# Optimization experiments

Measured on AMD Instinct MI355X. Metric: run time of the kernel, lower is better.

Reference implementation:

```python
import jax, jax.numpy as jnp
import numpy as np

B, NK, NQ = 16, 1024, 1024
D_IN, D_V, D_H = 3, 8, 128
NUGGET = 1e-3   # diagonal regularizer for the kriging covariance solve
EPS = 1e-12     # keeps sqrt differentiable at zero distance


def _mlp(x, w1, b1, w2, b2, w3, b3):
    # Linear -> ReLU -> Linear -> ReLU -> Linear (torch Linear: y = x @ W.T + b)
    h = jax.nn.relu(x @ w1.T + b1)
    h = jax.nn.relu(h @ w2.T + b2)
    return h @ w3.T + b3


def _cdist(a, b):
    # a: [B,N,D], b: [B,M,D] -> [B,N,M] Euclidean distances
    d2 = (jnp.sum(a * a, -1)[:, :, None]
          + jnp.sum(b * b, -1)[:, None, :]
          - 2.0 * jnp.einsum('bnd,bmd->bnm', a, b))
    return jnp.sqrt(jnp.maximum(d2, 0.0) + EPS)


def _linear_init(key, out_f, in_f):
    k1, k2 = jax.random.split(key)
    lim = 1.0 / np.sqrt(in_f)
    w = jax.random.uniform(k1, (out_f, in_f), jnp.float32, -lim, lim)
    b = jax.random.uniform(k2, (out_f,), jnp.float32, -lim, lim)
    return w, b


def setup_inputs() -> dict:
    key = jax.random.key(0)
    ks = jax.random.split(key, 10)
    KEY = jax.random.normal(ks[0], (B, NK, D_IN), jnp.float32)
    VALUE = jax.random.normal(ks[1], (B, NK, D_V), jnp.float32)
    QUERY = jax.random.normal(ks[2], (B, NQ, D_IN), jnp.float32)
    W1_w, W1_b = _linear_init(ks[3], D_H, D_IN)
    W2_w, W2_b = _linear_init(ks[4], D_H, D_H)
    W3_w, W3_b = _linear_init(ks[5], D_IN, D_H)
    Wv1_w, Wv1_b = _linear_init(ks[6], D_H, D_V)
    Wv2_w, Wv2_b = _linear_init(ks[7], D_H, D_H)
    Wv3_w, Wv3_b = _linear_init(ks[8], D_V, D_H)
    return dict(KEY=KEY, VALUE=VALUE, QUERY=QUERY,
                W1_w=W1_w, W1_b=W1_b, W2_w=W2_w, W2_b=W2_b, W3_w=W3_w, W3_b=W3_b,
                Wv1_w=Wv1_w, Wv1_b=Wv1_b, Wv2_w=Wv2_w, Wv2_b=Wv2_b, Wv3_w=Wv3_w, Wv3_b=Wv3_b)


def reference(KEY, VALUE, QUERY,
              W1_w, W1_b, W2_w, W2_b, W3_w, W3_b,
              Wv1_w, Wv1_b, Wv2_w, Wv2_b, Wv3_w, Wv3_b):
    # shared MLP on KEY and QUERY, separate MLP on VALUE
    Wk = _mlp(KEY, W1_w, W1_b, W2_w, W2_b, W3_w, W3_b)
    Wq = _mlp(QUERY, W1_w, W1_b, W2_w, W2_b, W3_w, W3_b)
    Wv = _mlp(VALUE, Wv1_w, Wv1_b, Wv2_w, Wv2_b, Wv3_w, Wv3_b)
    VALUE_scale = VALUE * Wv                  # einsum('bij,bij->bij')
    # kriging prediction with learned elementwise coordinate scalings
    Ks = KEY * Wk                             # [B,NK,D_IN]
    Qs = QUERY * Wq                           # [B,NQ,D_IN]
    C_kk = jnp.exp(-_cdist(Ks, Ks)) + NUGGET * jnp.eye(NK, dtype=KEY.dtype)  # [B,NK,NK]
    C_qk = jnp.exp(-_cdist(Qs, Ks))                                          # [B,NQ,NK]
    # kriging weights: solve C_kk @ lam = C_qk^T  -> lam [B,NK,NQ]
    lam = jnp.linalg.solve(C_kk, jnp.swapaxes(C_qk, 1, 2))
    # prediction: weighted sum of scaled values -> [B,NQ,D_V]
    return jnp.einsum('bkq,bkv->bqv', lam, VALUE_scale)
```

## Files before the change

### kernel.cpp

```cpp
#include <hip/hip_runtime.h>
#include <hip/hip_bf16.h>


__device__ __forceinline__ int row_of(int e) {
    int i = (int)((sqrtf(8.0f * (float)e + 1.0f) - 1.0f) * 0.5f);
    while ((i + 1) * (i + 2) / 2 <= e) i++;
    while (i * (i + 1) / 2 > e) i--;
    return i;
}

__global__ void k_transpose(const float* __restrict__ W2, const float* __restrict__ Wv2,
                            float* __restrict__ W2T, float* __restrict__ Wv2T) {
    int tid = blockIdx.x * 256 + threadIdx.x;
    int e = tid & 16383;
    int r = e >> 7, c = e & 127;
    if (tid < 16384) W2T[c * 128 + r] = W2[e];
    else             Wv2T[c * 128 + r] = Wv2[e];
}

template<int DI, int P>
__device__ __forceinline__ void mlp_body(const float* __restrict__ in,
                                         float* __restrict__ out, int base,
                                         const float* __restrict__ W1,
                                         const float* __restrict__ b1,
                                         const float* __restrict__ W2T,
                                         const float* __restrict__ b2,
                                         const float* __restrict__ W3,
                                         const float* __restrict__ b3) {
    __shared__ float xs[P][DI];
    __shared__ float h1[P][128];
    __shared__ float h2[P][129];
    int t = threadIdx.x;
    for (int i = t; i < P * DI; i += 128) xs[i / DI][i % DI] = in[base * DI + i];
    __syncthreads();
    float w1r[DI];
#pragma unroll
    for (int d = 0; d < DI; d++) w1r[d] = W1[t * DI + d];
    float b1t = b1[t], b2t = b2[t];
#pragma unroll
    for (int p = 0; p < P; p++) {
        float s = b1t;
#pragma unroll
        for (int d = 0; d < DI; d++) s += w1r[d] * xs[p][d];
        h1[p][t] = fmaxf(s, 0.0f);
    }
    __syncthreads();
    float acc[P];
#pragma unroll
    for (int p = 0; p < P; p++) acc[p] = b2t;
    for (int k = 0; k < 128; k++) {
        float w = W2T[k * 128 + t];
#pragma unroll
        for (int p = 0; p < P; p++) acc[p] += w * h1[p][k];
    }
#pragma unroll
    for (int p = 0; p < P; p++) h2[p][t] = fmaxf(acc[p], 0.0f);
    __syncthreads();
    if (t < P * DI) {
        int p = t / DI, d = t % DI;
        float s = b3[d];
        for (int k = 0; k < 128; k++) s += W3[d * 128 + k] * h2[p][k];
        int gi = base * DI + t;
        out[gi] = in[gi] * s;
    }
}

__global__ void k_mlp_kq(const float* __restrict__ KEY, float* __restrict__ Ks,
                         const float* __restrict__ QUERY, float* __restrict__ Qs,
                         const float* __restrict__ W1, const float* __restrict__ b1,
                         const float* __restrict__ W2T, const float* __restrict__ b2,
                         const float* __restrict__ W3, const float* __restrict__ b3) {
    if (blockIdx.x < 512)
        mlp_body<3, 32>(KEY, Ks, blockIdx.x * 32, W1, b1, W2T, b2, W3, b3);
    else
        mlp_body<3, 32>(QUERY, Qs, (blockIdx.x - 512) * 32, W1, b1, W2T, b2, W3, b3);
}

__global__ void k_mlp_v(const float* __restrict__ VALUE, float* __restrict__ Vs,
                        const float* __restrict__ W1, const float* __restrict__ b1,
                        const float* __restrict__ W2T, const float* __restrict__ b2,
                        const float* __restrict__ W3, const float* __restrict__ b3) {
    mlp_body<8, 16>(VALUE, Vs, blockIdx.x * 16, W1, b1, W2T, b2, W3, b3);
}

__global__ void k_buildC(const float* __restrict__ Ks, float* __restrict__ C) {
    long idx = (long)blockIdx.x * 256 + threadIdx.x;
    int b = (int)(idx >> 20);
    int rem = (int)(idx & 1048575);
    int i = rem >> 10, j = rem & 1023;
    const float* a = Ks + ((long)b * 1024 + i) * 3;
    const float* bb = Ks + ((long)b * 1024 + j) * 3;
    float d0 = a[0] - bb[0], d1 = a[1] - bb[1], d2 = a[2] - bb[2];
    float dist = sqrtf(d0 * d0 + d1 * d1 + d2 * d2 + 1e-12f);
    float v = __expf(-dist);
    if (i == j) v += 1e-3f;
    C[idx] = v;
}

__device__ void potf_body(float* __restrict__ C, float* __restrict__ V,
                          float* smem, int o, int last, int b) {
    int tid = threadIdx.x;
    float* A = C + (long)b * 1048576;
    float* Vp = V + (long)b * 8192;
    float (*T)[132]      = (float(*)[132])smem;
    float (*cv)[8]       = (float(*)[8])(smem + 16896);
    float (*cw)[8]       = (float(*)[8])(smem + 17920);
    float (*Pn)[8]       = (float(*)[8])(smem + 18944);
    float (*St)[32][132] = (float(*)[32][132])(smem + 19968);
    float (*Lc)[32][33]  = (float(*)[32][33])(smem + 19968);
    float* rsd           = smem + 28416;
    float (*Wb)[32][36]  = (float(*)[32][36])(smem + 28544);
    float (*zs)[9]       = (float(*)[9])(smem + 30848);

    bool active = (tid < 272);
    int ti = 0, tj = 0, hh = 0;
    if (active) { int e = tid >> 1; hh = tid & 1; ti = row_of(e); tj = e - ti * (ti + 1) / 2; }
    int r0 = ti * 8 + hh * 4, c0t = tj * 8;
    int lane = tid & 63;
    int sr = tid >> 2, slk = (tid & 3) * 8;

    if (o > 0) {
        const float* sp = A + (long)(o + sr) * 1024 + (o - 128) + slk;
        float4 v0 = *(const float4*)sp;
        float4 v1 = *(const float4*)(sp + 4);
        St[0][slk    ][sr] = v0.x; St[0][slk + 1][sr] = v0.y;
        St[0][slk + 2][sr] = v0.z; St[0][slk + 3][sr] = v0.w;
        St[0][slk + 4][sr] = v1.x; St[0][slk + 5][sr] = v1.y;
        St[0][slk + 6][sr] = v1.z; St[0][slk + 7][sr] = v1.w;
    }
    float Treg[4][8];
    if (active) {
        const float* src = A + (long)(o + r0) * 1024 + o + c0t;
#pragma unroll
        for (int i = 0; i < 4; i++) {
            float4 va = *(const float4*)(src + (long)i * 1024);
            float4 vb = *(const float4*)(src + (long)i * 1024 + 4);
            Treg[i][0] = va.x; Treg[i][1] = va.y; Treg[i][2] = va.z; Treg[i][3] = va.w;
            Treg[i][4] = vb.x; Treg[i][5] = vb.y; Treg[i][6] = vb.z; Treg[i][7] = vb.w;
        }
    }
    if (o > 0) {
        for (int kc = 0; kc < 4; kc++) {
            __syncthreads();
            if (kc < 3) {
                const float* sp = A + (long)(o + sr) * 1024 + (o - 128) + (kc + 1) * 32 + slk;
                float4 v0 = *(const float4*)sp;
                float4 v1 = *(const float4*)(sp + 4);
                int nb = (kc + 1) & 1;
                St[nb][slk    ][sr] = v0.x; St[nb][slk + 1][sr] = v0.y;
                St[nb][slk + 2][sr] = v0.z; St[nb][slk + 3][sr] = v0.w;
                St[nb][slk + 4][sr] = v1.x; St[nb][slk + 5][sr] = v1.y;
                St[nb][slk + 6][sr] = v1.z; St[nb][slk + 7][sr] = v1.w;
            }
            if (active) {
                int buf = kc & 1;
#pragma unroll 4
                for (int k = 0; k < 32; k++) {
                    float4 a0 = *(const float4*)&St[buf][k][r0];
                    float4 b0 = *(const float4*)&St[buf][k][c0t];
                    float4 b1 = *(const float4*)&St[buf][k][c0t + 4];
                    float aa[4] = {a0.x, a0.y, a0.z, a0.w};
                    float bb[8] = {b0.x, b0.y, b0.z, b0.w, b1.x, b1.y, b1.z, b1.w};
#pragma unroll
                    for (int i = 0; i < 4; i++)
#pragma unroll
                        for (int j = 0; j < 8; j++) Treg[i][j] -= aa[i] * bb[j];
                }
            }
        }
    }
    if (active && tj == 0) {
#pragma unroll
        for (int i = 0; i < 4; i++) {
            *(float4*)&Pn[r0 + i][0] = make_float4(Treg[i][0], Treg[i][1], Treg[i][2], Treg[i][3]);
            *(float4*)&Pn[r0 + i][4] = make_float4(Treg[i][4], Treg[i][5], Treg[i][6], Treg[i][7]);
        }
    }
    __syncthreads();
    for (int jbt = 0; jbt < 16; jbt++) {
        int jb = jbt * 8;
        if (tid < 64) {
            int r1 = lane, r2 = 64 + lane;
            float v1[8], v2[8], w1[8], w2[8];
#pragma unroll
            for (int q = 0; q < 8; q++) {
                int j = jb + q;
                int jl = j & 63;
                bool hi = (j >= 64);
                float a1 = Pn[r1][q], a2 = Pn[r2][q];
#pragma unroll
                for (int p = 0; p < 8; p++) {
                    if (p < q) {
                        float wj = __shfl(hi ? w2[p] : w1[p], jl);
                        a1 -= v1[p] * wj;
                        a2 -= v2[p] * wj;
                    }
                }
                v1[q] = a1; v2[q] = a2;
                float dj = __shfl(hi ? a2 : a1, jl);
                float dinv = 1.0f / dj;
                w1[q] = a1 * dinv; w2[q] = a2 * dinv;
            }
            *(float4*)&cv[r1][0] = make_float4(v1[0], v1[1], v1[2], v1[3]);
            *(float4*)&cv[r1][4] = make_float4(v1[4], v1[5], v1[6], v1[7]);
            *(float4*)&cv[r2][0] = make_float4(v2[0], v2[1], v2[2], v2[3]);
            *(float4*)&cv[r2][4] = make_float4(v2[4], v2[5], v2[6], v2[7]);
            *(float4*)&cw[r1][0] = make_float4(w1[0], w1[1], w1[2], w1[3]);
            *(float4*)&cw[r1][4] = make_float4(w1[4], w1[5], w1[6], w1[7]);
            *(float4*)&cw[r2][0] = make_float4(w2[0], w2[1], w2[2], w2[3]);
            *(float4*)&cw[r2][4] = make_float4(w2[4], w2[5], w2[6], w2[7]);
        }
        __syncthreads();
        if (active && tj == jbt) {
#pragma unroll
            for (int i = 0; i < 4; i++) {
                float4 va = *(const float4*)&cv[r0 + i][0];
                float4 vb = *(const float4*)&cv[r0 + i][4];
                Treg[i][0] = va.x; Treg[i][1] = va.y; Treg[i][2] = va.z; Treg[i][3] = va.w;
                Treg[i][4] = vb.x; Treg[i][5] = vb.y; Treg[i][6] = vb.z; Treg[i][7] = vb.w;
            }
        } else if (active && tj > jbt) {
#pragma unroll
            for (int h = 0; h < 2; h++) {
                float va4[4][4], wb4[8][4];
#pragma unroll
                for (int i = 0; i < 4; i++) {
                    float4 v = *(const float4*)&cv[r0 + i][h * 4];
                    va4[i][0] = v.x; va4[i][1] = v.y; va4[i][2] = v.z; va4[i][3] = v.w;
                }
#pragma unroll
                for (int j = 0; j < 8; j++) {
                    float4 v = *(const float4*)&cw[c0t + j][h * 4];
                    wb4[j][0] = v.x; wb4[j][1] = v.y; wb4[j][2] = v.z; wb4[j][3] = v.w;
                }
#pragma unroll
                for (int i = 0; i < 4; i++)
#pragma unroll
                    for (int j = 0; j < 8; j++)
                        Treg[i][j] -= va4[i][0] * wb4[j][0] + va4[i][1] * wb4[j][1]
                                    + va4[i][2] * wb4[j][2] + va4[i][3] * wb4[j][3];
            }
            if (tj == jbt + 1) {
#pragma unroll
                for (int i = 0; i < 4; i++) {
                    *(float4*)&Pn[r0 + i][0] = make_float4(Treg[i][0], Treg[i][1], Treg[i][2], Treg[i][3]);
                    *(float4*)&Pn[r0 + i][4] = make_float4(Treg[i][4], Treg[i][5], Treg[i][6], Treg[i][7]);
                }
            }
        }
        __syncthreads();
    }
    if (active) {
#pragma unroll
        for (int i = 0; i < 4; i++) {
            *(float4*)&T[r0 + i][c0t]     = make_float4(Treg[i][0], Treg[i][1], Treg[i][2], Treg[i][3]);
            *(float4*)&T[r0 + i][c0t + 4] = make_float4(Treg[i][4], Treg[i][5], Treg[i][6], Treg[i][7]);
        }
    }
    __syncthreads();
    if (tid < 128) rsd[tid] = rsqrtf(T[tid][tid]);
    __syncthreads();
    {
        int rg = tid >> 5, cg = tid & 31;
#pragma unroll
        for (int j = 0; j < 4; j++) {
            int c = cg + 32 * j;
#pragma unroll
            for (int i = 0; i < 8; i++) {
                int r = rg * 8 + i;
                if (c <= r) T[r][c] *= rsd[c];
                else        T[r][c] = 0.0f;
            }
        }
    }
    __syncthreads();
    {
        int wv = tid >> 6;
        if (wv < 4 && lane < 32) {
            int d0 = wv * 32;
            int j = lane;
            float x[32];
#pragma unroll
            for (int i = 0; i < 32; i++) {
                float dinv = 1.0f / T[d0 + i][d0 + i];
                float s = 0.0f;
#pragma unroll
                for (int k = 0; k < i; k++) s += T[d0 + i][d0 + k] * x[k];
                x[i] = (i == j) ? dinv : -s * dinv;
            }
#pragma unroll
            for (int i = 0; i < 32; i++) T[d0 + i][d0 + j] = x[i];
        }
        if (tid >= 256) {
            for (int idx = tid - 256; idx < 6144; idx += 256) {
                int p = idx >> 10;
                int e = idx & 1023;
                int r = e >> 5, c = e & 31;
                int i3 = (p == 0) ? 1 : (p <= 2 ? 2 : 3);
                int kb = (p == 0) ? 0 : (p <= 2 ? p - 1 : p - 3);
                Lc[p][r][c] = T[i3 * 32 + r][kb * 32 + c];
            }
        }
    }
    __syncthreads();
    {
        int team = tid >> 8, ttid = tid & 255;
        int orr = ttid >> 3, oc = (ttid & 7) * 4;
        for (int st = 0; st < 3; st++) {
            int i3, j3;
            if (team == 0) { i3 = st + 1; j3 = 0; }
            else           { i3 = (st == 0) ? 2 : 3; j3 = (st == 2) ? 2 : 1; }
            float w0 = 0, w1 = 0, w2 = 0, w3 = 0;
            for (int kb = j3; kb < i3; kb++) {
                int p = i3 * (i3 - 1) / 2 + kb;
#pragma unroll 8
                for (int kk = 0; kk < 32; kk++) {
                    float l = Lc[p][orr][kk];
                    float4 t = *(const float4*)&T[kb * 32 + kk][j3 * 32 + oc];
                    w0 += l * t.x; w1 += l * t.y; w2 += l * t.z; w3 += l * t.w;
                }
            }
            *(float4*)&Wb[team][orr][oc] = make_float4(w0, w1, w2, w3);
            __syncthreads();
            float v0 = 0, v1 = 0, v2 = 0, v3 = 0;
#pragma unroll 8
            for (int kk = 0; kk < 32; kk++) {
                float l = T[i3 * 32 + orr][i3 * 32 + kk];
                float4 wv = *(const float4*)&Wb[team][kk][oc];
                v0 += l * wv.x; v1 += l * wv.y; v2 += l * wv.z; v3 += l * wv.w;
            }
            T[i3 * 32 + orr][j3 * 32 + oc    ] = -v0;
            T[i3 * 32 + orr][j3 * 32 + oc + 1] = -v1;
            T[i3 * 32 + orr][j3 * 32 + oc + 2] = -v2;
            T[i3 * 32 + orr][j3 * 32 + oc + 3] = -v3;
            __syncthreads();
        }
    }
    {
        int r = tid >> 2, c0 = (tid & 3) * 32;
        float* dst = A + (long)(o + r) * 1024 + o + c0;
#pragma unroll
        for (int k = 0; k < 8; k++) {
            int c = c0 + 4 * k;
            *(float4*)(dst + 4 * k) = make_float4(T[r][c], T[r][c + 1], T[r][c + 2], T[r][c + 3]);
        }
    }
    {
        int k = tid >> 2, c2 = (tid & 3) * 2;
        float2 v = *(const float2*)&Vp[(o + k) * 8 + c2];
        zs[k][c2] = v.x; zs[k][c2 + 1] = v.y;
    }
    __syncthreads();
    {
        int r = tid & 127, c2 = (tid >> 7) * 2;
        float y0 = 0, y1 = 0;
#pragma unroll 8
        for (int k = 0; k < 128; k++) {
            float l = T[r][k];
            y0 += l * zs[k][c2];
            y1 += l * zs[k][c2 + 1];
        }
        if (!last) {
            *(float2*)&Vp[(o + r) * 8 + c2] = make_float2(y0, y1);
        } else {
            __syncthreads();
            zs[r][c2] = y0; zs[r][c2 + 1] = y1;
            __syncthreads();
            float x0 = 0, x1 = 0;
#pragma unroll 8
            for (int k = 0; k < 128; k++) {
                float l = T[k][r];
                x0 += l * zs[k][c2];
                x1 += l * zs[k][c2 + 1];
            }
            *(float2*)&Vp[(o + r) * 8 + c2] = make_float2(x0, x1);
        }
    }
}

__device__ void syrk_body(float* __restrict__ C, float* smem,
                          int o, int pti, int ptj, int b) {
    float* A = C + (long)b * 1048576;
    int bi = o + 128 + pti * 128, bj = o + 128 + ptj * 128;
    float (*As)[132] = (float(*)[132])smem;
    float (*Bs)[132] = (float(*)[132])(smem + 4224);
    int tid = threadIdx.x;
    int tx = tid & 15, ty = tid >> 4;
    float acc[4][8] = {};
    int lr = tid >> 2;
    int lk = (tid & 3) * 8;
    bool diag = (bi == bj);
    for (int kc = 0; kc < 128; kc += 32) {
        {
            const float* src = A + (long)(bi + lr) * 1024 + o + kc + lk;
            float4 v0 = *(const float4*)src;
            float4 v1 = *(const float4*)(src + 4);
            As[lk    ][lr] = v0.x; As[lk + 1][lr] = v0.y;
            As[lk + 2][lr] = v0.z; As[lk + 3][lr] = v0.w;
            As[lk + 4][lr] = v1.x; As[lk + 5][lr] = v1.y;
            As[lk + 6][lr] = v1.z; As[lk + 7][lr] = v1.w;
            if (!diag) {
                const float* sb = A + (long)(bj + lr) * 1024 + o + kc + lk;
                float4 w0 = *(const float4*)sb;
                float4 w1 = *(const float4*)(sb + 4);
                Bs[lk    ][lr] = w0.x; Bs[lk + 1][lr] = w0.y;
                Bs[lk + 2][lr] = w0.z; Bs[lk + 3][lr] = w0.w;
                Bs[lk + 4][lr] = w1.x; Bs[lk + 5][lr] = w1.y;
                Bs[lk + 6][lr] = w1.z; Bs[lk + 7][lr] = w1.w;
            }
        }
        __syncthreads();
        {
            float (*Bp)[132] = diag ? As : Bs;
#pragma unroll
            for (int k = 0; k < 32; k++) {
                float4 a0 = *(const float4*)&As[k][ty * 4];
                float4 b0 = *(const float4*)&Bp[k][tx * 8];
                float4 b1 = *(const float4*)&Bp[k][tx * 8 + 4];
                float aa[4] = {a0.x, a0.y, a0.z, a0.w};
                float bb[8] = {b0.x, b0.y, b0.z, b0.w, b1.x, b1.y, b1.z, b1.w};
#pragma unroll
                for (int i = 0; i < 4; i++)
#pragma unroll
                    for (int j = 0; j < 8; j++) acc[i][j] += aa[i] * bb[j];
            }
        }
        __syncthreads();
    }
#pragma unroll
    for (int i = 0; i < 4; i++) {
        int r = bi + ty * 4 + i;
        float* dst = A + (long)r * 1024 + bj + tx * 8;
        if (!diag) {
            float4 p0 = *(const float4*)dst;
            float4 p1 = *(const float4*)(dst + 4);
            p0.x -= acc[i][0]; p0.y -= acc[i][1]; p0.z -= acc[i][2]; p0.w -= acc[i][3];
            p1.x -= acc[i][4]; p1.y -= acc[i][5]; p1.z -= acc[i][6]; p1.w -= acc[i][7];
            *(float4*)dst = p0;
            *(float4*)(dst + 4) = p1;
        } else {
#pragma unroll
            for (int j = 0; j < 8; j++) {
                int c = bj + tx * 8 + j;
                if (c <= r) dst[j] -= acc[i][j];
            }
        }
    }
}

__global__ __launch_bounds__(512) void k_potf_syrk(float* __restrict__ C,
                                                   float* __restrict__ V,
                                                   int o, int last) {
    __shared__ __align__(16) float smem[32000];
    int bx = blockIdx.x;
    if (bx < 16) {
        potf_body(C, V, smem, o, last, bx);
    } else {
        int v = bx - 16;
        int bb = v & 15;
        int p = (v >> 4) + 1;
        int tii = row_of(p);
        int tjj = p - tii * (tii + 1) / 2;
        syrk_body(C, smem, o - 128, tii, tjj, bb);
    }
}

__global__ __launch_bounds__(512) void k_trsmg(float* __restrict__ C,
                                               float* __restrict__ V, int o) {
    int b = blockIdx.y;
    float* A = C + (long)b * 1048576;
    float* Vp = V + (long)b * 8192;
    int bi = o + 128 + blockIdx.x * 128;
    const float* Linv = A + (long)o * 1024 + o;
    __shared__ float As[32][132];
    __shared__ float Ls[32][132];
    int tid = threadIdx.x;
    int tx = tid & 15, ty = tid >> 4;
    float acc[4][8] = {};
    int lr = tid >> 2;
    int lk = (tid & 3) * 8;
    for (int kc = 0; kc < 128; kc += 32) {
        {
            const float* src = A + (long)(bi + lr) * 1024 + o + kc + lk;
            const float* sl  = Linv + (long)lr * 1024 + kc + lk;
            float4 v0 = *(const float4*)src;
            float4 v1 = *(const float4*)(src + 4);
            As[lk    ][lr] = v0.x; As[lk + 1][lr] = v0.y;
            As[lk + 2][lr] = v0.z; As[lk + 3][lr] = v0.w;
            As[lk + 4][lr] = v1.x; As[lk + 5][lr] = v1.y;
            As[lk + 6][lr] = v1.z; As[lk + 7][lr] = v1.w;
            float4 w0 = *(const float4*)sl;
            float4 w1 = *(const float4*)(sl + 4);
            Ls[lk    ][lr] = w0.x; Ls[lk + 1][lr] = w0.y;
            Ls[lk + 2][lr] = w0.z; Ls[lk + 3][lr] = w0.w;
            Ls[lk + 4][lr] = w1.x; Ls[lk + 5][lr] = w1.y;
            Ls[lk + 6][lr] = w1.z; Ls[lk + 7][lr] = w1.w;
        }
        __syncthreads();
#pragma unroll
        for (int k = 0; k < 32; k++) {
            float4 a0 = *(const float4*)&As[k][ty * 4];
            float4 b0 = *(const float4*)&Ls[k][tx * 8];
            float4 b1 = *(const float4*)&Ls[k][tx * 8 + 4];
            float aa[4] = {a0.x, a0.y, a0.z, a0.w};
            float bb[8] = {b0.x, b0.y, b0.z, b0.w, b1.x, b1.y, b1.z, b1.w};
#pragma unroll
            for (int i = 0; i < 4; i++)
#pragma unroll
                for (int j = 0; j < 8; j++) acc[i][j] += aa[i] * bb[j];
        }
        __syncthreads();
    }
#pragma unroll
    for (int i = 0; i < 4; i++) {
        float* dst = A + (long)(bi + ty * 4 + i) * 1024 + o + tx * 8;
        *(float4*)dst       = make_float4(acc[i][0], acc[i][1], acc[i][2], acc[i][3]);
        *(float4*)(dst + 4) = make_float4(acc[i][4], acc[i][5], acc[i][6], acc[i][7]);
    }
    float* ysf = &Ls[0][0];
    {
        int k = tid >> 2, c2 = (tid & 3) * 2;
        float2 v = *(const float2*)&Vp[(o + k) * 8 + c2];
        ysf[k * 9 + c2] = v.x; ysf[k * 9 + c2 + 1] = v.y;
    }
    __syncthreads();
    float zacc0 = 0, zacc1 = 0;
    int zr = tid & 127, zc0 = (tid >> 7) * 2;
#pragma unroll
    for (int ch = 0; ch < 4; ch++) {
        if ((tx >> 2) == ch) {
            int cb = (tx & 3) * 8;
#pragma unroll
            for (int j = 0; j < 8; j++)
#pragma unroll
                for (int i = 0; i < 4; i++)
                    As[cb + j][ty * 4 + i] = acc[i][j];
        }
        __syncthreads();
#pragma unroll 8
        for (int k = 0; k < 32; k++) {
            float l = As[k][zr];
            const float* yp = &ysf[(ch * 32 + k) * 9 + zc0];
            zacc0 += l * yp[0]; zacc1 += l * yp[1];
        }
        __syncthreads();
    }
    float* vp = &Vp[(bi + zr) * 8 + zc0];
    float2 old = *(const float2*)vp;
    old.x -= zacc0; old.y -= zacc1;
    *(float2*)vp = old;
}

__global__ __launch_bounds__(512) void k_bstep(const float* __restrict__ C,
                                               float* __restrict__ V, int k) {
    int b = blockIdx.y, j = blockIdx.x, tid = threadIdx.x;
    const float* A = C + (long)b * 1048576;
    float* Vp = V + (long)b * 8192;
    __shared__ float Lb[128][129];
    __shared__ float xs[128][9];
    __shared__ float ys[128][9];
    {
        int kk = tid >> 2, c2 = (tid & 3) * 2;
        float2 v = *(const float2*)&Vp[(k * 128 + kk) * 8 + c2];
        xs[kk][c2] = v.x; xs[kk][c2 + 1] = v.y;
    }
#pragma unroll
    for (int m = 0; m < 8; m++) {
        int e = tid + m * 512;
        int i = e >> 5, j4 = (e & 31) * 4;
        float4 v = *(const float4*)&A[(long)(k * 128 + i) * 1024 + j * 128 + j4];
        Lb[i][j4] = v.x; Lb[i][j4+1] = v.y; Lb[i][j4+2] = v.z; Lb[i][j4+3] = v.w;
    }
    __syncthreads();
    int r = tid & 127, c2 = (tid >> 7) * 2;
    float u0 = 0, u1 = 0;
#pragma unroll 8
    for (int kk = 0; kk < 128; kk++) {
        float l = Lb[kk][r];
        u0 += l * xs[kk][c2];
        u1 += l * xs[kk][c2 + 1];
    }
    float* vp = &Vp[(j * 128 + r) * 8 + c2];
    float2 old = *(const float2*)vp;
    old.x -= u0; old.y -= u1;
    if (j < k - 1) {
        *(float2*)vp = old;
    } else {
        ys[r][c2] = old.x; ys[r][c2 + 1] = old.y;
        __syncthreads();
        int o = j * 128;
#pragma unroll
        for (int m = 0; m < 8; m++) {
            int e = tid + m * 512;
            int i = e >> 5, j4 = (e & 31) * 4;
            float4 v = *(const float4*)&A[(long)(o + i) * 1024 + o + j4];
            Lb[i][j4] = v.x; Lb[i][j4+1] = v.y; Lb[i][j4+2] = v.z; Lb[i][j4+3] = v.w;
        }
        __syncthreads();
        float x0 = 0, x1 = 0;
#pragma unroll 8
        for (int kk = 0; kk < 128; kk++) {
            float l = Lb[kk][r];
            x0 += l * ys[kk][c2];
            x1 += l * ys[kk][c2 + 1];
        }
        *(float2*)vp = make_float2(x0, x1);
    }
}

__global__ void k_out(const float* __restrict__ Qs, const float* __restrict__ Ks,
                      const float* __restrict__ X, float* __restrict__ out) {
    int b = blockIdx.x >> 4;
    int qc = blockIdx.x & 15;
    int t = threadIdx.x;
    int q = t & 63, ks = t >> 6;
    __shared__ float kx[1024][3];
    __shared__ __align__(16) float xv[1024][8];
    __shared__ float red[4][64][8];
    for (int i = t; i < 3072; i += 256) kx[i / 3][i % 3] = Ks[b * 3072 + i];
    for (int i = t; i < 8192; i += 256) xv[i >> 3][i & 7] = X[b * 8192 + i];
    __syncthreads();
    int gq = b * 1024 + qc * 64 + q;
    const float* qp = Qs + (long)gq * 3;
    float qx = qp[0], qy = qp[1], qz = qp[2];
    float acc[8] = {};
    int k0 = ks * 256;
#pragma unroll 2
    for (int k = k0; k < k0 + 256; k++) {
        float dx = qx - kx[k][0], dy = qy - kx[k][1], dz = qz - kx[k][2];
        float w = __expf(-sqrtf(dx * dx + dy * dy + dz * dz + 1e-12f));
        float4 xa = *(const float4*)&xv[k][0];
        float4 xb = *(const float4*)&xv[k][4];
        acc[0] += w * xa.x; acc[1] += w * xa.y; acc[2] += w * xa.z; acc[3] += w * xa.w;
        acc[4] += w * xb.x; acc[5] += w * xb.y; acc[6] += w * xb.z; acc[7] += w * xb.w;
    }
#pragma unroll
    for (int c = 0; c < 8; c++) red[ks][q][c] = acc[c];
    __syncthreads();
    if (ks == 0) {
        float* op = out + (long)gq * 8;
#pragma unroll
        for (int c = 0; c < 8; c++)
            op[c] = red[0][q][c] + red[1][q][c] + red[2][q][c] + red[3][q][c];
    }
}

extern "C" void kernel_launch(void* const* d_in, const int* in_sizes, int n_in,
                              void* d_out, int out_size, void* d_ws, size_t ws_size,
                              hipStream_t stream) {
    const float* KEY   = (const float*)d_in[0];
    const float* VALUE = (const float*)d_in[1];
    const float* QUERY = (const float*)d_in[2];
    const float* W1w = (const float*)d_in[3];  const float* W1b = (const float*)d_in[4];
    const float* W2w = (const float*)d_in[5];  const float* W2b = (const float*)d_in[6];
    const float* W3w = (const float*)d_in[7];  const float* W3b = (const float*)d_in[8];
    const float* Wv1w = (const float*)d_in[9]; const float* Wv1b = (const float*)d_in[10];
    const float* Wv2w = (const float*)d_in[11];const float* Wv2b = (const float*)d_in[12];
    const float* Wv3w = (const float*)d_in[13];const float* Wv3b = (const float*)d_in[14];

    float* ws  = (float*)d_ws;
    float* C    = ws;
    float* Ks   = C + 16777216;
    float* Qs   = Ks + 49152;
    float* Vs   = Qs + 49152;
    float* W2T  = Vs + 131072;
    float* Wv2T = W2T + 16384;

    float* out = (float*)d_out;

    hipLaunchKernelGGL(k_transpose, dim3(128), dim3(256), 0, stream, W2w, Wv2w, W2T, Wv2T);
    hipLaunchKernelGGL(k_mlp_kq, dim3(1024), dim3(128), 0, stream,
                       KEY, Ks, QUERY, Qs, W1w, W1b, W2T, W2b, W3w, W3b);
    hipLaunchKernelGGL(k_mlp_v, dim3(1024), dim3(128), 0, stream,
                       VALUE, Vs, Wv1w, Wv1b, Wv2T, Wv2b, Wv3w, Wv3b);
    hipLaunchKernelGGL(k_buildC, dim3(65536), dim3(256), 0, stream, Ks, C);

    for (int s = 0; s < 8; s++) {
        int o = s * 128;
        int np = 0;
        if (s >= 1) { int ntp = 8 - s; np = ntp * (ntp + 1) / 2 - 1; }
        hipLaunchKernelGGL(k_potf_syrk, dim3(16 + np * 16), dim3(512), 0, stream,
                           C, Vs, o, (s == 7) ? 1 : 0);
        int nt = 7 - s;
        if (nt > 0)
            hipLaunchKernelGGL(k_trsmg, dim3(nt, 16), dim3(512), 0, stream, C, Vs, o);
    }
    for (int k = 7; k >= 1; k--)
        hipLaunchKernelGGL(k_bstep, dim3(k, 16), dim3(512), 0, stream, C, Vs, k);

    hipLaunchKernelGGL(k_out, dim3(256), dim3(256), 0, stream, Qs, Ks, Vs, out);
}
```

Measured before the change: 973.0 us.

## Fuse backward-substitution steps into a single persistent kernel per batch

```diff
diff --git a/kernel.cpp b/kernel.cpp
--- a/kernel.cpp
+++ b/kernel.cpp
@@ -551,49 +551,46 @@
     *(float2*)vp = old;
 }
 
-__global__ __launch_bounds__(512) void k_bstep(const float* __restrict__ C,
-                                               float* __restrict__ V, int k) {
-    int b = blockIdx.y, j = blockIdx.x, tid = threadIdx.x;
+__global__ __launch_bounds__(512) void k_bsolve(const float* __restrict__ C,
+                                                float* __restrict__ V) {
+    int b = blockIdx.x, tid = threadIdx.x;
     const float* A = C + (long)b * 1048576;
     float* Vp = V + (long)b * 8192;
     __shared__ float Lb[128][129];
     __shared__ float xs[128][9];
-    __shared__ float ys[128][9];
-    {
-        int kk = tid >> 2, c2 = (tid & 3) * 2;
-        float2 v = *(const float2*)&Vp[(k * 128 + kk) * 8 + c2];
-        xs[kk][c2] = v.x; xs[kk][c2 + 1] = v.y;
-    }
-#pragma unroll
-    for (int m = 0; m < 8; m++) {
-        int e = tid + m * 512;
-        int i = e >> 5, j4 = (e & 31) * 4;
-        float4 v = *(const float4*)&A[(long)(k * 128 + i) * 1024 + j * 128 + j4];
-        Lb[i][j4] = v.x; Lb[i][j4+1] = v.y; Lb[i][j4+2] = v.z; Lb[i][j4+3] = v.w;
-    }
-    __syncthreads();
     int r = tid & 127, c2 = (tid >> 7) * 2;
-    float u0 = 0, u1 = 0;
+    for (int k = 6; k >= 0; k--) {
+        float2 acc = *(const float2*)&Vp[(k * 128 + r) * 8 + c2];
+        for (int m = 7; m > k; m--) {
+            {
+                int kk = tid >> 2, cc = (tid & 3) * 2;
+                float2 v = *(const float2*)&Vp[(m * 128 + kk) * 8 + cc];
+                xs[kk][cc] = v.x; xs[kk][cc + 1] = v.y;
+            }
+#pragma unroll
+            for (int mm = 0; mm < 8; mm++) {
+                int e = tid + mm * 512;
+                int i = e >> 5, j4 = (e & 31) * 4;
+                float4 v = *(const float4*)&A[(long)(m * 128 + i) * 1024 + k * 128 + j4];
+                Lb[i][j4] = v.x; Lb[i][j4+1] = v.y; Lb[i][j4+2] = v.z; Lb[i][j4+3] = v.w;
+            }
+            __syncthreads();
+            float u0 = 0, u1 = 0;
 #pragma unroll 8
-    for (int kk = 0; kk < 128; kk++) {
-        float l = Lb[kk][r];
-        u0 += l * xs[kk][c2];
-        u1 += l * xs[kk][c2 + 1];
-    }
-    float* vp = &Vp[(j * 128 + r) * 8 + c2];
-    float2 old = *(const float2*)vp;
-    old.x -= u0; old.y -= u1;
-    if (j < k - 1) {
-        *(float2*)vp = old;
-    } else {
-        ys[r][c2] = old.x; ys[r][c2 + 1] = old.y;
-        __syncthreads();
-        int o = j * 128;
-#pragma unroll
-        for (int m = 0; m < 8; m++) {
-            int e = tid + m * 512;
+            for (int kk = 0; kk < 128; kk++) {
+                float l = Lb[kk][r];
+                u0 += l * xs[kk][c2];
+                u1 += l * xs[kk][c2 + 1];
+            }
+            acc.x -= u0; acc.y -= u1;
+            __syncthreads();
+        }
+        xs[r][c2] = acc.x; xs[r][c2 + 1] = acc.y;
+#pragma unroll
+        for (int mm = 0; mm < 8; mm++) {
+            int e = tid + mm * 512;
             int i = e >> 5, j4 = (e & 31) * 4;
-            float4 v = *(const float4*)&A[(long)(o + i) * 1024 + o + j4];
+            float4 v = *(const float4*)&A[(long)(k * 128 + i) * 1024 + k * 128 + j4];
             Lb[i][j4] = v.x; Lb[i][j4+1] = v.y; Lb[i][j4+2] = v.z; Lb[i][j4+3] = v.w;
         }
         __syncthreads();
@@ -601,10 +598,11 @@
 #pragma unroll 8
         for (int kk = 0; kk < 128; kk++) {
             float l = Lb[kk][r];
-            x0 += l * ys[kk][c2];
-            x1 += l * ys[kk][c2 + 1];
-        }
-        *(float2*)vp = make_float2(x0, x1);
+            x0 += l * xs[kk][c2];
+            x1 += l * xs[kk][c2 + 1];
+        }
+        *(float2*)&Vp[(k * 128 + r) * 8 + c2] = make_float2(x0, x1);
+        __syncthreads();
     }
 }
 
@@ -685,8 +683,7 @@
         if (nt > 0)
             hipLaunchKernelGGL(k_trsmg, dim3(nt, 16), dim3(512), 0, stream, C, Vs, o);
     }
-    for (int k = 7; k >= 1; k--)
-        hipLaunchKernelGGL(k_bstep, dim3(k, 16), dim3(512), 0, stream, C, Vs, k);
+    hipLaunchKernelGGL(k_bsolve, dim3(16), dim3(512), 0, stream, C, Vs);
 
     hipLaunchKernelGGL(k_out, dim3(256), dim3(256), 0, stream, Qs, Ks, Vs, out);
 }
```

After: 1.071 ms. +10.1%, slower.

## Defer forward-substitution RHS updates into next potf/syrk launch and merge MLP kernels

Applied to the files above, without the earlier changes.

```diff
diff --git a/kernel.cpp b/kernel.cpp
--- a/kernel.cpp
+++ b/kernel.cpp
@@ -65,22 +65,22 @@
     }
 }
 
-__global__ void k_mlp_kq(const float* __restrict__ KEY, float* __restrict__ Ks,
-                         const float* __restrict__ QUERY, float* __restrict__ Qs,
-                         const float* __restrict__ W1, const float* __restrict__ b1,
-                         const float* __restrict__ W2T, const float* __restrict__ b2,
-                         const float* __restrict__ W3, const float* __restrict__ b3) {
-    if (blockIdx.x < 512)
-        mlp_body<3, 32>(KEY, Ks, blockIdx.x * 32, W1, b1, W2T, b2, W3, b3);
+__global__ void k_mlp(const float* __restrict__ KEY, float* __restrict__ Ks,
+                      const float* __restrict__ QUERY, float* __restrict__ Qs,
+                      const float* __restrict__ VALUE, float* __restrict__ Vs,
+                      const float* __restrict__ W1, const float* __restrict__ b1,
+                      const float* __restrict__ W2T, const float* __restrict__ b2,
+                      const float* __restrict__ W3, const float* __restrict__ b3,
+                      const float* __restrict__ Wv1, const float* __restrict__ bv1,
+                      const float* __restrict__ Wv2T, const float* __restrict__ bv2,
+                      const float* __restrict__ Wv3, const float* __restrict__ bv3) {
+    int bx = blockIdx.x;
+    if (bx < 512)
+        mlp_body<3, 32>(KEY, Ks, bx * 32, W1, b1, W2T, b2, W3, b3);
+    else if (bx < 1024)
+        mlp_body<3, 32>(QUERY, Qs, (bx - 512) * 32, W1, b1, W2T, b2, W3, b3);
     else
-        mlp_body<3, 32>(QUERY, Qs, (blockIdx.x - 512) * 32, W1, b1, W2T, b2, W3, b3);
-}
-
-__global__ void k_mlp_v(const float* __restrict__ VALUE, float* __restrict__ Vs,
-                        const float* __restrict__ W1, const float* __restrict__ b1,
-                        const float* __restrict__ W2T, const float* __restrict__ b2,
-                        const float* __restrict__ W3, const float* __restrict__ b3) {
-    mlp_body<8, 16>(VALUE, Vs, blockIdx.x * 16, W1, b1, W2T, b2, W3, b3);
+        mlp_body<8, 16>(VALUE, Vs, (bx - 1024) * 16, Wv1, bv1, Wv2T, bv2, Wv3, bv3);
 }
 
 __global__ void k_buildC(const float* __restrict__ Ks, float* __restrict__ C) {
@@ -111,6 +111,7 @@
     float* rsd           = smem + 28416;
     float (*Wb)[32][36]  = (float(*)[32][36])(smem + 28544);
     float (*zs)[9]       = (float(*)[9])(smem + 30848);
+    float (*ysP)[9]      = (float(*)[9])(smem + 30848);
 
     bool active = (tid < 272);
     int ti = 0, tj = 0, hh = 0;
@@ -119,6 +120,7 @@
     int lane = tid & 63;
     int sr = tid >> 2, slk = (tid & 3) * 8;
 
+    float zinit[8], zpart[8];
     if (o > 0) {
         const float* sp = A + (long)(o + sr) * 1024 + (o - 128) + slk;
         float4 v0 = *(const float4*)sp;
@@ -127,6 +129,22 @@
         St[0][slk + 2][sr] = v0.z; St[0][slk + 3][sr] = v0.w;
         St[0][slk + 4][sr] = v1.x; St[0][slk + 5][sr] = v1.y;
         St[0][slk + 6][sr] = v1.z; St[0][slk + 7][sr] = v1.w;
+        if (tid >= 256 && tid < 384) {
+            int r = tid - 256;
+            float4 a0 = *(const float4*)&Vp[(o - 128 + r) * 8];
+            float4 a1 = *(const float4*)&Vp[(o - 128 + r) * 8 + 4];
+            ysP[r][0] = a0.x; ysP[r][1] = a0.y; ysP[r][2] = a0.z; ysP[r][3] = a0.w;
+            ysP[r][4] = a1.x; ysP[r][5] = a1.y; ysP[r][6] = a1.z; ysP[r][7] = a1.w;
+        }
+        if (tid >= 384) {
+            int r = tid - 384;
+            float4 a0 = *(const float4*)&Vp[(o + r) * 8];
+            float4 a1 = *(const float4*)&Vp[(o + r) * 8 + 4];
+            zinit[0] = a0.x; zinit[1] = a0.y; zinit[2] = a0.z; zinit[3] = a0.w;
+            zinit[4] = a1.x; zinit[5] = a1.y; zinit[6] = a1.z; zinit[7] = a1.w;
+#pragma unroll
+            for (int c = 0; c < 8; c++) zpart[c] = 0.0f;
+        }
     }
     float Treg[4][8];
     if (active) {
@@ -165,6 +183,15 @@
                     for (int i = 0; i < 4; i++)
 #pragma unroll
                         for (int j = 0; j < 8; j++) Treg[i][j] -= aa[i] * bb[j];
+                }
+            } else if (tid >= 384) {
+                int r = tid - 384;
+                int buf = kc & 1;
+#pragma unroll 4
+                for (int k = 0; k < 32; k++) {
+                    float lp = St[buf][k][r];
+#pragma unroll
+                    for (int c = 0; c < 8; c++) zpart[c] += lp * ysP[kc * 32 + k][c];
                 }
             }
         }
@@ -345,10 +372,16 @@
             *(float4*)(dst + 4 * k) = make_float4(T[r][c], T[r][c + 1], T[r][c + 2], T[r][c + 3]);
         }
     }
-    {
-        int k = tid >> 2, c2 = (tid & 3) * 2;
-        float2 v = *(const float2*)&Vp[(o + k) * 8 + c2];
-        zs[k][c2] = v.x; zs[k][c2 + 1] = v.y;
+    if (o > 0) {
+        if (tid >= 384) {
+            int r = tid - 384;
+#pragma unroll
+            for (int c = 0; c < 8; c++) zs[r][c] = zinit[c] - zpart[c];
+        }
+    } else {
+        int k = tid >> 2, c2v = (tid & 3) * 2;
+        float2 v = *(const float2*)&Vp[(o + k) * 8 + c2v];
+        zs[k][c2v] = v.x; zs[k][c2v + 1] = v.y;
     }
     __syncthreads();
     {
@@ -448,20 +481,61 @@
     }
 }
 
+__device__ void zupd_body(const float* __restrict__ C, float* __restrict__ V,
+                          float* smem, int o1, int m, int b) {
+    const float* A = C + (long)b * 1048576;
+    float* Vp = V + (long)b * 8192;
+    float (*Lb)[129] = (float(*)[129])smem;
+    float (*ys)[9]   = (float(*)[9])(smem + 16512);
+    int tid = threadIdx.x;
+    int o0 = o1 - 128;
+    {
+        int kk = tid >> 2, cc = (tid & 3) * 2;
+        float2 v = *(const float2*)&Vp[(o0 + kk) * 8 + cc];
+        ys[kk][cc] = v.x; ys[kk][cc + 1] = v.y;
+    }
+#pragma unroll
+    for (int mm = 0; mm < 8; mm++) {
+        int e = tid + mm * 512;
+        int i = e >> 5, j4 = (e & 31) * 4;
+        float4 v = *(const float4*)&A[(long)(m * 128 + i) * 1024 + o0 + j4];
+        Lb[i][j4] = v.x; Lb[i][j4+1] = v.y; Lb[i][j4+2] = v.z; Lb[i][j4+3] = v.w;
+    }
+    __syncthreads();
+    int r = tid & 127, c2 = (tid >> 7) * 2;
+    float u0 = 0, u1 = 0;
+#pragma unroll 8
+    for (int kk = 0; kk < 128; kk++) {
+        float l = Lb[r][kk];
+        u0 += l * ys[kk][c2];
+        u1 += l * ys[kk][c2 + 1];
+    }
+    float* vp = &Vp[(m * 128 + r) * 8 + c2];
+    float2 old = *(const float2*)vp;
+    old.x -= u0; old.y -= u1;
+    *(float2*)vp = old;
+}
+
 __global__ __launch_bounds__(512) void k_potf_syrk(float* __restrict__ C,
                                                    float* __restrict__ V,
-                                                   int o, int last) {
+                                                   int o, int last, int nsy) {
     __shared__ __align__(16) float smem[32000];
     int bx = blockIdx.x;
     if (bx < 16) {
         potf_body(C, V, smem, o, last, bx);
-    } else {
+    } else if (bx < 16 + nsy) {
         int v = bx - 16;
         int bb = v & 15;
         int p = (v >> 4) + 1;
         int tii = row_of(p);
         int tjj = p - tii * (tii + 1) / 2;
         syrk_body(C, smem, o - 128, tii, tjj, bb);
+    } else {
+        int v = bx - 16 - nsy;
+        int bb = v & 15;
+        int zj = v >> 4;
+        int m = (o >> 7) + 1 + zj;
+        zupd_body(C, V, smem, o, m, bb);
     }
 }
 
@@ -469,7 +543,6 @@
                                                float* __restrict__ V, int o) {
     int b = blockIdx.y;
     float* A = C + (long)b * 1048576;
-    float* Vp = V + (long)b * 8192;
     int bi = o + 128 + blockIdx.x * 128;
     const float* Linv = A + (long)o * 1024 + o;
     __shared__ float As[32][132];
@@ -517,38 +590,6 @@
         *(float4*)dst       = make_float4(acc[i][0], acc[i][1], acc[i][2], acc[i][3]);
         *(float4*)(dst + 4) = make_float4(acc[i][4], acc[i][5], acc[i][6], acc[i][7]);
     }
-    float* ysf = &Ls[0][0];
-    {
-        int k = tid >> 2, c2 = (tid & 3) * 2;
-        float2 v = *(const float2*)&Vp[(o + k) * 8 + c2];
-        ysf[k * 9 + c2] = v.x; ysf[k * 9 + c2 + 1] = v.y;
-    }
-    __syncthreads();
-    float zacc0 = 0, zacc1 = 0;
-    int zr = tid & 127, zc0 = (tid >> 7) * 2;
-#pragma unroll
-    for (int ch = 0; ch < 4; ch++) {
-        if ((tx >> 2) == ch) {
-            int cb = (tx & 3) * 8;
-#pragma unroll
-            for (int j = 0; j < 8; j++)
-#pragma unroll
-                for (int i = 0; i < 4; i++)
-                    As[cb + j][ty * 4 + i] = acc[i][j];
-        }
-        __syncthreads();
-#pragma unroll 8
-        for (int k = 0; k < 32; k++) {
-            float l = As[k][zr];
-            const float* yp = &ysf[(ch * 32 + k) * 9 + zc0];
-            zacc0 += l * yp[0]; zacc1 += l * yp[1];
-        }
-        __syncthreads();
-    }
-    float* vp = &Vp[(bi + zr) * 8 + zc0];
-    float2 old = *(const float2*)vp;
-    old.x -= zacc0; old.y -= zacc1;
-    *(float2*)vp = old;
 }
 
 __global__ __launch_bounds__(512) void k_bstep(const float* __restrict__ C,
@@ -669,18 +710,19 @@
     float* out = (float*)d_out;
 
     hipLaunchKernelGGL(k_transpose, dim3(128), dim3(256), 0, stream, W2w, Wv2w, W2T, Wv2T);
-    hipLaunchKernelGGL(k_mlp_kq, dim3(1024), dim3(128), 0, stream,
-                       KEY, Ks, QUERY, Qs, W1w, W1b, W2T, W2b, W3w, W3b);
-    hipLaunchKernelGGL(k_mlp_v, dim3(1024), dim3(128), 0, stream,
-                       VALUE, Vs, Wv1w, Wv1b, Wv2T, Wv2b, Wv3w, Wv3b);
+    hipLaunchKernelGGL(k_mlp, dim3(2048), dim3(128), 0, stream,
+                       KEY, Ks, QUERY, Qs, VALUE, Vs,
+                       W1w, W1b, W2T, W2b, W3w, W3b,
+                       Wv1w, Wv1b, Wv2T, Wv2b, Wv3w, Wv3b);
     hipLaunchKernelGGL(k_buildC, dim3(65536), dim3(256), 0, stream, Ks, C);
 
     for (int s = 0; s < 8; s++) {
         int o = s * 128;
         int np = 0;
         if (s >= 1) { int ntp = 8 - s; np = ntp * (ntp + 1) / 2 - 1; }
-        hipLaunchKernelGGL(k_potf_syrk, dim3(16 + np * 16), dim3(512), 0, stream,
-                           C, Vs, o, (s == 7) ? 1 : 0);
+        int nz = (s >= 1) ? (7 - s) : 0;
+        hipLaunchKernelGGL(k_potf_syrk, dim3(16 + np * 16 + nz * 16), dim3(512), 0, stream,
+                           C, Vs, o, (s == 7) ? 1 : 0, np * 16);
         int nt = 7 - s;
         if (nt > 0)
             hipLaunchKernelGGL(k_trsmg, dim3(nt, 16), dim3(512), 0, stream, C, Vs, o);
```

New measurement: 950.6 us. 1.02x faster.
